# Optimization experiments

Measured on AMD Instinct MI355X. Metric: run time of the kernel, lower is better.

Reference implementation:

```python
import jax, jax.numpy as jnp
import numpy as np

D_MODEL = 768
NUM_HEADS = 12
D_K = D_MODEL // NUM_HEADS


def setup_inputs() -> dict:
    key = jax.random.key(0)
    ks = jax.random.split(key, 11)
    B, L = 1, 4096
    s = 1.0 / np.sqrt(D_MODEL)
    return {
        "q": jax.random.normal(ks[0], (B, L, D_MODEL), jnp.float32),
        "k": jax.random.normal(ks[1], (B, L, D_MODEL), jnp.float32),
        "v": jax.random.normal(ks[2], (B, L, D_MODEL), jnp.float32),
        "Wq": jax.random.normal(ks[3], (D_MODEL, D_MODEL), jnp.float32) * s,
        "bq": jax.random.normal(ks[4], (D_MODEL,), jnp.float32) * s,
        "Wk": jax.random.normal(ks[5], (D_MODEL, D_MODEL), jnp.float32) * s,
        "bk": jax.random.normal(ks[6], (D_MODEL,), jnp.float32) * s,
        "Wv": jax.random.normal(ks[7], (D_MODEL, D_MODEL), jnp.float32) * s,
        "bv": jax.random.normal(ks[8], (D_MODEL,), jnp.float32) * s,
        "Wo": jax.random.normal(ks[9], (D_MODEL, D_MODEL), jnp.float32) * s,
        "bo": jax.random.normal(ks[10], (D_MODEL,), jnp.float32) * s,
    }


def reference(q, k, v, Wq, bq, Wk, bk, Wv, bv, Wo, bo):
    B, L, _ = q.shape
    # linear projections (torch Linear: x @ W.T + b)
    qp = q @ Wq.T + bq
    kp = k @ Wk.T + bk
    vp = v @ Wv.T + bv
    # split heads: (B, H, L, d_k)
    def split(x):
        return x.reshape(B, L, NUM_HEADS, D_K).transpose(0, 2, 1, 3)
    qh, kh, vh = split(qp), split(kp), split(vp)
    scale = 1.0 / jnp.sqrt(jnp.asarray(D_K, qh.dtype))
    scores = jnp.einsum("bhqd,bhkd->bhqk", qh, kh) * scale  # (B,H,L,L)
    weights = jax.nn.softmax(scores, axis=-1)
    out = jnp.einsum("bhqk,bhkd->bhqd", weights, vh)
    out = out.transpose(0, 2, 1, 3).reshape(B, L, D_MODEL)
    return out @ Wo.T + bo
```

## Files before the change

### kernel.cpp

```cpp
#include <hip/hip_runtime.h>
#include <stdint.h>
#include <math.h>

#define L_SEQ  4096
#define DMODEL 768
#define NHEADS 12
#define DKH    64
#define QSCALE 0.18033688011112042f

typedef _Float16 f16;
typedef __attribute__((ext_vector_type(8))) _Float16 half8;
typedef __attribute__((ext_vector_type(4))) _Float16 half4;
typedef __attribute__((ext_vector_type(4))) float f32x4;
typedef __attribute__((ext_vector_type(4))) float fv4;
typedef __attribute__((ext_vector_type(16))) float f32x16;
typedef __attribute__((ext_vector_type(4))) unsigned int uint4v;

#define MFMA16(a, b, c) __builtin_amdgcn_mfma_f32_16x16x32_f16(a, b, c, 0, 0, 0)
#define MFMA32(a, b, c) __builtin_amdgcn_mfma_f32_32x32x16_f16(a, b, c, 0, 0, 0)

#define NE ((size_t)L_SEQ * DMODEL)
#define WE ((size_t)DMODEL * DMODEL)

static __device__ __forceinline__ unsigned int pack2(float a, float b) {
  return __builtin_bit_cast(unsigned int, __builtin_amdgcn_cvt_pkrtz(a, b));
}

__global__ __launch_bounds__(256)
void cvt_w(const float* __restrict__ Wq, const float* __restrict__ Wk,
           const float* __restrict__ Wv, const float* __restrict__ Wo,
           f16* __restrict__ w16)
{
  const size_t WE4 = WE / 4;
  size_t i = (size_t)blockIdx.x * 256 + threadIdx.x;
  const float* srcs[4] = {Wq, Wk, Wv, Wo};
  int r = (int)(i / WE4);
  size_t off = i - (size_t)r * WE4;
  float4 f = reinterpret_cast<const float4*>(srcs[r])[off];
  half4 h; h[0] = (f16)f.x; h[1] = (f16)f.y; h[2] = (f16)f.z; h[3] = (f16)f.w;
  reinterpret_cast<half4*>(w16 + (size_t)r * WE)[off] = h;
}

__global__ __launch_bounds__(256)
void qkv_gemm(const float* __restrict__ xq, const float* __restrict__ xk,
              const float* __restrict__ xv, const f16* __restrict__ w16,
              const float* __restrict__ bq, const float* __restrict__ bk,
              const float* __restrict__ bv,
              f16* __restrict__ Qp, f16* __restrict__ Kp, f16* __restrict__ VpT)
{
  __shared__ f16 As[128][72];
  __shared__ f16 Bs[64][72];
  const int tid  = threadIdx.x;
  const int lane = tid & 63, wid = tid >> 6;
  const int lq   = lane & 15, quad = lane >> 4;
  const int wm   = (wid & 1) * 64, wn = (wid >> 1) * 32;
  const int m0   = blockIdx.y * 128;
  const int widx = blockIdx.x / 12;
  const int n0   = (blockIdx.x % 12) * 64;
  const float* X = (widx == 0) ? xq : (widx == 1) ? xk : xv;
  const f16* W = w16 + (size_t)widx * WE;
  const float* Bv = (widx == 0) ? bq : (widx == 1) ? bk : bv;

  const int arow = tid >> 1, aseg = (tid & 1) * 32;
  const int brow = tid >> 2, bseg = (tid & 3) * 16;
  const float* aptr = X + (size_t)(m0 + arow) * DMODEL + aseg;
  const f16*   bptr = W + (size_t)(n0 + brow) * DMODEL + bseg;

  fv4 a4[8];
#pragma unroll
  for (int u = 0; u < 8; ++u) a4[u] = reinterpret_cast<const fv4*>(aptr)[u];
  half8 b0 = *reinterpret_cast<const half8*>(bptr);
  half8 b1 = *reinterpret_cast<const half8*>(bptr + 8);

  f32x4 acc[4][2] = {};

  for (int k0 = 0; k0 < DMODEL; k0 += 64) {
#pragma unroll
    for (int u = 0; u < 4; ++u) {
      half8 h;
#pragma unroll
      for (int e = 0; e < 4; ++e) {
        h[e]     = (f16)a4[2 * u][e];
        h[4 + e] = (f16)a4[2 * u + 1][e];
      }
      *reinterpret_cast<half8*>(&As[arow][aseg + u * 8]) = h;
    }
    *reinterpret_cast<half8*>(&Bs[brow][bseg])     = b0;
    *reinterpret_cast<half8*>(&Bs[brow][bseg + 8]) = b1;
    __syncthreads();

    if (k0 + 64 < DMODEL) {
#pragma unroll
      for (int u = 0; u < 8; ++u)
        a4[u] = reinterpret_cast<const fv4*>(aptr + k0 + 64)[u];
      b0 = *reinterpret_cast<const half8*>(bptr + k0 + 64);
      b1 = *reinterpret_cast<const half8*>(bptr + k0 + 72);
    }

#pragma unroll
    for (int ks = 0; ks < 2; ++ks) {
      half8 bf[2];
#pragma unroll
      for (int nf = 0; nf < 2; ++nf)
        bf[nf] = *reinterpret_cast<half8*>(&Bs[wn + nf * 16 + lq][ks * 32 + quad * 8]);
#pragma unroll
      for (int mf = 0; mf < 4; ++mf) {
        half8 af = *reinterpret_cast<half8*>(&As[wm + mf * 16 + lq][ks * 32 + quad * 8]);
#pragma unroll
        for (int nf = 0; nf < 2; ++nf)
          acc[mf][nf] = MFMA16(af, bf[nf], acc[mf][nf]);
      }
    }
    __syncthreads();
  }

#pragma unroll
  for (int nf = 0; nf < 2; ++nf) {
    const int col  = n0 + wn + nf * 16 + lq;
    const float bias = Bv[col];
#pragma unroll
    for (int mf = 0; mf < 4; ++mf) {
      const int rowb = m0 + wm + mf * 16 + quad * 4;
      if (widx == 2) {
        half4 o4;
#pragma unroll
        for (int r = 0; r < 4; ++r) o4[r] = (f16)(acc[mf][nf][r] + bias);
        *reinterpret_cast<half4*>(VpT + (size_t)col * L_SEQ + rowb) = o4;
      } else if (widx == 0) {
#pragma unroll
        for (int r = 0; r < 4; ++r)
          Qp[(size_t)(rowb + r) * DMODEL + col] = (f16)((acc[mf][nf][r] + bias) * QSCALE);
      } else {
#pragma unroll
        for (int r = 0; r < 4; ++r)
          Kp[(size_t)(rowb + r) * DMODEL + col] = (f16)(acc[mf][nf][r] + bias);
      }
    }
  }
}

__global__ __launch_bounds__(256, 3)
void attn_mfma4(const f16* __restrict__ Qp, const f16* __restrict__ Kp,
                const f16* __restrict__ VpT, f16* __restrict__ AO)
{
  const int h  = blockIdx.x;
  const int q0 = blockIdx.y * 64;
  const int tid  = threadIdx.x;
  const int lane = tid & 63, wid = tid >> 6;
  const int l31  = lane & 31, hc = lane >> 5;
  const int qh   = wid & 1, kh = wid >> 1;

  __shared__ __align__(16) char smem[36864];
  f16 (*Ks)[64][72] = (f16 (*)[64][72])smem;
  f16 (*Vt)[64][72] = (f16 (*)[64][72])(smem + 18432);
  float* Of  = (float*)smem;
  float* lf  = (float*)(smem + 16384);
  f16*   Of16 = (f16*)(smem + 16640);

  half8 qf[4];
#pragma unroll
  for (int st = 0; st < 4; ++st)
    qf[st] = *reinterpret_cast<const half8*>(
        Qp + (size_t)(q0 + qh * 32 + l31) * DMODEL + h * DKH + st * 16 + hc * 8);

  half8 ones;
#pragma unroll
  for (int e = 0; e < 8; ++e) ones[e] = (f16)1.0f;
  const f32x16 zf = {};

  f32x16 oacc[2] = {};
  f32x16 lacc = {};

  const int srow = tid >> 2, sseg = (tid & 3) * 16;
  const f16* kbase = Kp  + (size_t)srow * DMODEL + h * DKH + sseg;
  const f16* vbase = VpT + (size_t)(h * DKH + srow) * L_SEQ + sseg;

  half8 k0 = *reinterpret_cast<const half8*>(kbase);
  half8 k1 = *reinterpret_cast<const half8*>(kbase + 8);
  half8 v0 = *reinterpret_cast<const half8*>(vbase);
  half8 v1 = *reinterpret_cast<const half8*>(vbase + 8);
  *reinterpret_cast<half8*>(&Ks[0][srow][sseg])     = k0;
  *reinterpret_cast<half8*>(&Ks[0][srow][sseg + 8]) = k1;
  *reinterpret_cast<half8*>(&Vt[0][srow][sseg])     = v0;
  *reinterpret_cast<half8*>(&Vt[0][srow][sseg + 8]) = v1;
  k0 = *reinterpret_cast<const half8*>(kbase + (size_t)64 * DMODEL);
  k1 = *reinterpret_cast<const half8*>(kbase + (size_t)64 * DMODEL + 8);
  v0 = *reinterpret_cast<const half8*>(vbase + 64);
  v1 = *reinterpret_cast<const half8*>(vbase + 64 + 8);

  int p = 0;
#pragma unroll 2
  for (int kt = 0; kt < L_SEQ; kt += 64) {
    __syncthreads();

    if (kt + 64 < L_SEQ) {
      *reinterpret_cast<half8*>(&Ks[p ^ 1][srow][sseg])     = k0;
      *reinterpret_cast<half8*>(&Ks[p ^ 1][srow][sseg + 8]) = k1;
      *reinterpret_cast<half8*>(&Vt[p ^ 1][srow][sseg])     = v0;
      *reinterpret_cast<half8*>(&Vt[p ^ 1][srow][sseg + 8]) = v1;
    }
    if (kt + 128 < L_SEQ) {
      const f16* kn = kbase + (size_t)(kt + 128) * DMODEL;
      const f16* vn = vbase + (kt + 128);
      k0 = *reinterpret_cast<const half8*>(kn);
      k1 = *reinterpret_cast<const half8*>(kn + 8);
      v0 = *reinterpret_cast<const half8*>(vn);
      v1 = *reinterpret_cast<const half8*>(vn + 8);
    }

    __builtin_amdgcn_s_setprio(1);

    half8 kf0 = *reinterpret_cast<half8*>(&Ks[p][kh * 32 + l31][hc * 8]);
    f32x16 s = MFMA32(kf0, qf[0], zf);
#pragma unroll
    for (int st = 1; st < 4; ++st) {
      half8 kf = *reinterpret_cast<half8*>(&Ks[p][kh * 32 + l31][st * 16 + hc * 8]);
      s = MFMA32(kf, qf[st], s);
    }

    unsigned int pk[8];
#pragma unroll
    for (int i = 0; i < 8; ++i) {
      float p0 = __builtin_amdgcn_exp2f(s[2 * i]);
      float p1 = __builtin_amdgcn_exp2f(s[2 * i + 1]);
      pk[i] = pack2(p0, p1);
    }

#pragma unroll
    for (int st = 0; st < 2; ++st) {
      unsigned int w0 = pk[4 * st + 0], w1 = pk[4 * st + 1];
      unsigned int w2 = pk[4 * st + 2], w3 = pk[4 * st + 3];
      asm("v_permlane32_swap_b32 %0, %1" : "+v"(w0), "+v"(w2));
      asm("v_permlane32_swap_b32 %0, %1" : "+v"(w1), "+v"(w3));
      uint4v pw; pw[0] = w0; pw[1] = w1; pw[2] = w2; pw[3] = w3;
      half8 pf = __builtin_bit_cast(half8, pw);
      lacc = MFMA32(ones, pf, lacc);
#pragma unroll
      for (int a = 0; a < 2; ++a) {
        half8 vf = *reinterpret_cast<half8*>(&Vt[p][a * 32 + l31][kh * 32 + st * 16 + hc * 8]);
        oacc[a] = MFMA32(vf, pf, oacc[a]);
      }
    }
    __builtin_amdgcn_s_setprio(0);
    p ^= 1;
  }
  __syncthreads();

  const float lw = lacc[0];

  if (kh == 0) {
#pragma unroll
    for (int a = 0; a < 2; ++a)
#pragma unroll
      for (int r = 0; r < 16; ++r) {
        int d = a * 32 + (r & 3) + 8 * (r >> 2) + 4 * hc;
        Of[((qh * 64) + d) * 32 + l31] = oacc[a][r];
      }
    if (lane < 32) lf[qh * 32 + l31] = lw;
  }
  __syncthreads();
  if (kh == 1) {
    const float inv = 1.0f / (lf[qh * 32 + l31] + lw);
#pragma unroll
    for (int a = 0; a < 2; ++a)
#pragma unroll
      for (int r = 0; r < 16; ++r) {
        int d = a * 32 + (r & 3) + 8 * (r >> 2) + 4 * hc;
        float val = (Of[((qh * 64) + d) * 32 + l31] + oacc[a][r]) * inv;
        Of16[(qh * 32 + l31) * 64 + d] = (f16)val;
      }
  }
  __syncthreads();

  *reinterpret_cast<half8*>(AO + (size_t)(q0 + srow) * DMODEL + h * DKH + sseg) =
      *reinterpret_cast<half8*>(&Of16[srow * 64 + sseg]);
  *reinterpret_cast<half8*>(AO + (size_t)(q0 + srow) * DMODEL + h * DKH + sseg + 8) =
      *reinterpret_cast<half8*>(&Of16[srow * 64 + sseg + 8]);
}

__global__ __launch_bounds__(256)
void out_gemm(const f16* __restrict__ A, const f16* __restrict__ W,
              const float* __restrict__ Bv, float* __restrict__ O)
{
  __shared__ f16 As[64][72];
  __shared__ f16 Bs[64][72];
  const int tid  = threadIdx.x;
  const int lane = tid & 63, wid = tid >> 6;
  const int lq   = lane & 15, quad = lane >> 4;
  const int wm   = (wid & 1) * 32, wn = (wid >> 1) * 32;
  const int m0   = blockIdx.y * 64, n0 = blockIdx.x * 64;

  const int row = tid >> 2, seg = (tid & 3) * 16;
  const f16* aptr = A + (size_t)(m0 + row) * DMODEL + seg;
  const f16* bptr = W + (size_t)(n0 + row) * DMODEL + seg;

  half8 a0 = *reinterpret_cast<const half8*>(aptr);
  half8 a1 = *reinterpret_cast<const half8*>(aptr + 8);
  half8 b0 = *reinterpret_cast<const half8*>(bptr);
  half8 b1 = *reinterpret_cast<const half8*>(bptr + 8);

  f32x4 acc[2][2] = {};

  for (int k0 = 0; k0 < DMODEL; k0 += 64) {
    *reinterpret_cast<half8*>(&As[row][seg])     = a0;
    *reinterpret_cast<half8*>(&As[row][seg + 8]) = a1;
    *reinterpret_cast<half8*>(&Bs[row][seg])     = b0;
    *reinterpret_cast<half8*>(&Bs[row][seg + 8]) = b1;
    __syncthreads();

    if (k0 + 64 < DMODEL) {
      a0 = *reinterpret_cast<const half8*>(aptr + k0 + 64);
      a1 = *reinterpret_cast<const half8*>(aptr + k0 + 72);
      b0 = *reinterpret_cast<const half8*>(bptr + k0 + 64);
      b1 = *reinterpret_cast<const half8*>(bptr + k0 + 72);
    }

#pragma unroll
    for (int ks = 0; ks < 2; ++ks) {
      half8 bf[2];
#pragma unroll
      for (int nf = 0; nf < 2; ++nf)
        bf[nf] = *reinterpret_cast<half8*>(&Bs[wn + nf * 16 + lq][ks * 32 + quad * 8]);
#pragma unroll
      for (int mf = 0; mf < 2; ++mf) {
        half8 af = *reinterpret_cast<half8*>(&As[wm + mf * 16 + lq][ks * 32 + quad * 8]);
#pragma unroll
        for (int nf = 0; nf < 2; ++nf)
          acc[mf][nf] = MFMA16(af, bf[nf], acc[mf][nf]);
      }
    }
    __syncthreads();
  }

#pragma unroll
  for (int nf = 0; nf < 2; ++nf) {
    const int col = n0 + wn + nf * 16 + lq;
    const float bias = Bv[col];
#pragma unroll
    for (int mf = 0; mf < 2; ++mf) {
      const int rowb = m0 + wm + mf * 16 + quad * 4;
#pragma unroll
      for (int r = 0; r < 4; ++r)
        O[(size_t)(rowb + r) * DMODEL + col] = acc[mf][nf][r] + bias;
    }
  }
}

extern "C" void kernel_launch(void* const* d_in, const int* in_sizes, int n_in,
                              void* d_out, int out_size, void* d_ws, size_t ws_size,
                              hipStream_t stream) {
  const float* q  = (const float*)d_in[0];
  const float* k  = (const float*)d_in[1];
  const float* v  = (const float*)d_in[2];
  const float* Wq = (const float*)d_in[3];
  const float* bq = (const float*)d_in[4];
  const float* Wk = (const float*)d_in[5];
  const float* bk = (const float*)d_in[6];
  const float* Wv = (const float*)d_in[7];
  const float* bv = (const float*)d_in[8];
  const float* Wo = (const float*)d_in[9];
  const float* bo = (const float*)d_in[10];
  float* out = (float*)d_out;

  f16* w16 = (f16*)d_ws;
  f16* Qp  = w16 + 4 * WE;
  f16* Kp  = Qp + NE;
  f16* VpT = Kp + NE;
  f16* AO  = VpT + NE;

  const int ncvt = (int)(WE / 256);
  cvt_w<<<ncvt, 256, 0, stream>>>(Wq, Wk, Wv, Wo, w16);

  dim3 gqkv(36, L_SEQ / 128);
  qkv_gemm<<<gqkv, 256, 0, stream>>>(q, k, v, w16, bq, bk, bv, Qp, Kp, VpT);

  dim3 gattn(NHEADS, L_SEQ / 64);
  attn_mfma4<<<gattn, 256, 0, stream>>>(Qp, Kp, VpT, AO);

  dim3 gout(DMODEL / 64, L_SEQ / 64);
  out_gemm<<<gout, 256, 0, stream>>>(AO, w16 + 3 * WE, bo, out);
}
```

Baseline: 250.6 us.

## Swizzle GEMM block order and compute attention row sums with VALU adds

Both projection GEMMs move to a 1-D grid whose block index is remapped so that 8 consecutive blocks share an N column tile while walking different M tiles. This aims to improve L2/cache locality across XCD-interleaved dispatch. In attention, the extra MFMA with an all-ones operand that accumulated the softmax denominator is replaced by scalar adds of the exp values plus one cross-half shuffle, which frees MFMA issue slots. The K/V register prefetch is also shortened from two tiles ahead to one, and the unroll pragma is dropped. That may expose more global load latency in exchange for fewer live registers.

```diff
diff --git a/kernel.cpp b/kernel.cpp
--- a/kernel.cpp
+++ b/kernel.cpp
@@ -54,9 +54,16 @@
   const int lane = tid & 63, wid = tid >> 6;
   const int lq   = lane & 15, quad = lane >> 4;
   const int wm   = (wid & 1) * 64, wn = (wid >> 1) * 32;
-  const int m0   = blockIdx.y * 128;
-  const int widx = blockIdx.x / 12;
-  const int n0   = (blockIdx.x % 12) * 64;
+
+  const int d   = blockIdx.x;
+  const int r8  = d & 7;
+  const int j   = d >> 3;
+  const int g   = r8 + 8 * (j / 12);
+  const int nb  = j % 12;
+  const int widx = g / 32;
+  const int m0   = (g % 32) * 128;
+  const int n0   = nb * 64;
+
   const float* X = (widx == 0) ? xq : (widx == 1) ? xk : xv;
   const f16* W = w16 + (size_t)widx * WE;
   const float* Bv = (widx == 0) ? bq : (widx == 1) ? bk : bv;
@@ -163,13 +170,8 @@
     qf[st] = *reinterpret_cast<const half8*>(
         Qp + (size_t)(q0 + qh * 32 + l31) * DMODEL + h * DKH + st * 16 + hc * 8);
 
-  half8 ones;
-#pragma unroll
-  for (int e = 0; e < 8; ++e) ones[e] = (f16)1.0f;
-  const f32x16 zf = {};
-
   f32x16 oacc[2] = {};
-  f32x16 lacc = {};
+  float lsum = 0.0f;
 
   const int srow = tid >> 2, sseg = (tid & 3) * 16;
   const f16* kbase = Kp  + (size_t)srow * DMODEL + h * DKH + sseg;
@@ -179,29 +181,18 @@
   half8 k1 = *reinterpret_cast<const half8*>(kbase + 8);
   half8 v0 = *reinterpret_cast<const half8*>(vbase);
   half8 v1 = *reinterpret_cast<const half8*>(vbase + 8);
-  *reinterpret_cast<half8*>(&Ks[0][srow][sseg])     = k0;
-  *reinterpret_cast<half8*>(&Ks[0][srow][sseg + 8]) = k1;
-  *reinterpret_cast<half8*>(&Vt[0][srow][sseg])     = v0;
-  *reinterpret_cast<half8*>(&Vt[0][srow][sseg + 8]) = v1;
-  k0 = *reinterpret_cast<const half8*>(kbase + (size_t)64 * DMODEL);
-  k1 = *reinterpret_cast<const half8*>(kbase + (size_t)64 * DMODEL + 8);
-  v0 = *reinterpret_cast<const half8*>(vbase + 64);
-  v1 = *reinterpret_cast<const half8*>(vbase + 64 + 8);
 
   int p = 0;
-#pragma unroll 2
   for (int kt = 0; kt < L_SEQ; kt += 64) {
+    *reinterpret_cast<half8*>(&Ks[p][srow][sseg])     = k0;
+    *reinterpret_cast<half8*>(&Ks[p][srow][sseg + 8]) = k1;
+    *reinterpret_cast<half8*>(&Vt[p][srow][sseg])     = v0;
+    *reinterpret_cast<half8*>(&Vt[p][srow][sseg + 8]) = v1;
     __syncthreads();
 
     if (kt + 64 < L_SEQ) {
-      *reinterpret_cast<half8*>(&Ks[p ^ 1][srow][sseg])     = k0;
-      *reinterpret_cast<half8*>(&Ks[p ^ 1][srow][sseg + 8]) = k1;
-      *reinterpret_cast<half8*>(&Vt[p ^ 1][srow][sseg])     = v0;
-      *reinterpret_cast<half8*>(&Vt[p ^ 1][srow][sseg + 8]) = v1;
-    }
-    if (kt + 128 < L_SEQ) {
-      const f16* kn = kbase + (size_t)(kt + 128) * DMODEL;
-      const f16* vn = vbase + (kt + 128);
+      const f16* kn = kbase + (size_t)(kt + 64) * DMODEL;
+      const f16* vn = vbase + (kt + 64);
       k0 = *reinterpret_cast<const half8*>(kn);
       k1 = *reinterpret_cast<const half8*>(kn + 8);
       v0 = *reinterpret_cast<const half8*>(vn);
@@ -210,10 +201,9 @@
 
     __builtin_amdgcn_s_setprio(1);
 
-    half8 kf0 = *reinterpret_cast<half8*>(&Ks[p][kh * 32 + l31][hc * 8]);
-    f32x16 s = MFMA32(kf0, qf[0], zf);
-#pragma unroll
-    for (int st = 1; st < 4; ++st) {
+    f32x16 s = {};
+#pragma unroll
+    for (int st = 0; st < 4; ++st) {
       half8 kf = *reinterpret_cast<half8*>(&Ks[p][kh * 32 + l31][st * 16 + hc * 8]);
       s = MFMA32(kf, qf[st], s);
     }
@@ -223,6 +213,7 @@
     for (int i = 0; i < 8; ++i) {
       float p0 = __builtin_amdgcn_exp2f(s[2 * i]);
       float p1 = __builtin_amdgcn_exp2f(s[2 * i + 1]);
+      lsum += p0 + p1;
       pk[i] = pack2(p0, p1);
     }
 
@@ -234,7 +225,6 @@
       asm("v_permlane32_swap_b32 %0, %1" : "+v"(w1), "+v"(w3));
       uint4v pw; pw[0] = w0; pw[1] = w1; pw[2] = w2; pw[3] = w3;
       half8 pf = __builtin_bit_cast(half8, pw);
-      lacc = MFMA32(ones, pf, lacc);
 #pragma unroll
       for (int a = 0; a < 2; ++a) {
         half8 vf = *reinterpret_cast<half8*>(&Vt[p][a * 32 + l31][kh * 32 + st * 16 + hc * 8]);
@@ -246,7 +236,7 @@
   }
   __syncthreads();
 
-  const float lw = lacc[0];
+  float lw = lsum + __shfl_xor(lsum, 32);
 
   if (kh == 0) {
 #pragma unroll
@@ -288,7 +278,13 @@
   const int lane = tid & 63, wid = tid >> 6;
   const int lq   = lane & 15, quad = lane >> 4;
   const int wm   = (wid & 1) * 32, wn = (wid >> 1) * 32;
-  const int m0   = blockIdx.y * 64, n0 = blockIdx.x * 64;
+
+  const int d   = blockIdx.x;
+  const int r8  = d & 7;
+  const int j   = d >> 3;
+  const int g   = r8 + 8 * (j / 12);
+  const int nb  = j % 12;
+  const int m0  = g * 64, n0 = nb * 64;
 
   const int row = tid >> 2, seg = (tid & 3) * 16;
   const f16* aptr = A + (size_t)(m0 + row) * DMODEL + seg;
@@ -371,12 +367,10 @@
   const int ncvt = (int)(WE / 256);
   cvt_w<<<ncvt, 256, 0, stream>>>(Wq, Wk, Wv, Wo, w16);
 
-  dim3 gqkv(36, L_SEQ / 128);
-  qkv_gemm<<<gqkv, 256, 0, stream>>>(q, k, v, w16, bq, bk, bv, Qp, Kp, VpT);
+  qkv_gemm<<<1152, 256, 0, stream>>>(q, k, v, w16, bq, bk, bv, Qp, Kp, VpT);
 
   dim3 gattn(NHEADS, L_SEQ / 64);
   attn_mfma4<<<gattn, 256, 0, stream>>>(Qp, Kp, VpT, AO);
 
-  dim3 gout(DMODEL / 64, L_SEQ / 64);
-  out_gemm<<<gout, 256, 0, stream>>>(AO, w16 + 3 * WE, bo, out);
-}
+  out_gemm<<<768, 256, 0, stream>>>(AO, w16 + 3 * WE, bo, out);
+}
```

Measured after the change: 241.3 us. 3.7% less time.
